# Optimization experiments

Hardware: AMD Instinct MI355X
Metric: run time of the kernel (lower is better)

## Reference

```python
import jax, jax.numpy as jnp
import numpy as np

KSIZE = 3
PAD = (KSIZE - 1) // 2
SIGMA = 0.15 * KSIZE + 0.35  # 0.8, used for BOTH spatial and range weights (as in source)


def gaussian_kernel(ksize, sigma):
    if sigma <= 0:
        sigma = 0.3 * ((ksize - 1) * 0.5 - 1) + 0.8
    xs = np.arange(ksize, dtype=np.float32) - ksize // 2
    k1 = np.exp(-xs ** 2 / (2.0 * sigma ** 2))
    k = k1[:, None] * k1[None, :]
    return jnp.asarray((k / k.sum()).astype(np.float32))


def setup_inputs() -> dict:
    key = jax.random.key(0)
    ks = jax.random.split(key, 5)
    B, C_in, H, W = 8, 256, 128, 128
    C2 = 128
    x1 = jax.random.normal(ks[0], (B, C_in, H, W), jnp.float32)
    x2 = jax.random.normal(ks[1], (B, C2, 2 * H, 2 * W), jnp.float32)
    # Conv2d(in_ch, 1, kernel_size=1): weight [out=1, in], bias [1]
    w1 = jax.random.normal(ks[2], (1, C_in), jnp.float32) / np.float32(np.sqrt(C_in))
    b1 = jnp.zeros((1,), jnp.float32)
    # ConvTranspose2d(1, 1, k=2, s=2): weight [2, 2], bias [1]
    wt = jax.random.normal(ks[3], (2, 2), jnp.float32) * 0.5
    bt = jnp.zeros((1,), jnp.float32)
    return {"x1": x1, "x2": x2, "w1": w1, "b1": b1, "wt": wt, "bt": bt}


def reference(x1, x2, w1, b1, wt, bt):
    # 1x1 conv: [B, C_in, H, W] -> [B, 1, H, W]
    y = jnp.einsum('bchw,oc->bohw', x1, w1) + b1[None, :, None, None]
    B, _, H, W = y.shape
    # ConvTranspose2d(1,1,k=2,s=2): out[2h+dh, 2w+dw] = y[h,w] * wt[dh,dw] + bt
    up = (y[:, :, :, None, :, None] * wt[None, None, None, :, None, :]).reshape(
        B, 1, 2 * H, 2 * W) + bt[None, :, None, None]
    Hu, Wu = 2 * H, 2 * W
    # reflect pad then extract ksize x ksize patches (unfold equivalent)
    xp = jnp.pad(up, ((0, 0), (0, 0), (PAD, PAD), (PAD, PAD)), mode='reflect')
    patches = jnp.stack(
        [xp[:, :, i:i + Hu, j:j + Wu] for i in range(KSIZE) for j in range(KSIZE)],
        axis=-1)  # [B, 1, Hu, Wu, K*K]
    w_space = gaussian_kernel(KSIZE, SIGMA).reshape(-1)  # [K*K]
    diff = patches - up[..., None]
    w_color = jnp.exp(-(diff ** 2) / (2.0 * SIGMA ** 2))
    weights = w_color * w_space  # joint bilateral weights
    filtered = (weights * patches).sum(-1) / weights.sum(-1)  # [B, 1, Hu, Wu]
    gate = jax.nn.sigmoid(filtered)
    return gate * x2 + x2
```

## Files before the change

kernel.cpp:

```cpp
#include <hip/hip_runtime.h>
#include <hip/hip_bf16.h>


#define B     8
#define CIN   256
#define H     128
#define W     128
#define C2    128
#define HU    256
#define WU    256

__global__ __launch_bounds__(256) void conv1x1_kernel(
    const float* __restrict__ x1, const float* __restrict__ w1,
    const float* __restrict__ b1, float* __restrict__ y)
{
    __shared__ float wsh[CIN];
    __shared__ float4 sred[256];
    int tid = threadIdx.x;
    wsh[tid] = w1[tid];
    __syncthreads();

    int b      = blockIdx.x >> 6;
    int hwbase = (blockIdx.x & 63) * 256;

    int q  = tid & 63;
    int cc = tid >> 6;

    const float4* p = (const float4*)(x1 + (size_t)b * CIN * H * W + hwbase) + q;
    const int cstride = H * W / 4;

    float4 acc = make_float4(0.f, 0.f, 0.f, 0.f);
    int c0 = cc * 64;
    #pragma unroll 8
    for (int k = 0; k < 64; ++k) {
        int c = c0 + k;
        float4 v = p[(size_t)c * cstride];
        float wv = wsh[c];
        acc.x += v.x * wv; acc.y += v.y * wv;
        acc.z += v.z * wv; acc.w += v.w * wv;
    }
    sred[tid] = acc;
    __syncthreads();

    if (cc == 0) {
        float4 a = sred[q], b2 = sred[q + 64], c2 = sred[q + 128], d2 = sred[q + 192];
        float bias = b1[0];
        float4 r;
        r.x = a.x + b2.x + c2.x + d2.x + bias;
        r.y = a.y + b2.y + c2.y + d2.y + bias;
        r.z = a.z + b2.z + c2.z + d2.z + bias;
        r.w = a.w + b2.w + c2.w + d2.w + bias;
        ((float4*)(y + (size_t)b * H * W + hwbase))[q] = r;
    }
}

__device__ __forceinline__ int refl(int i, int n) {
    return i < 0 ? -i : (i >= n ? 2 * n - 2 - i : i);
}

__global__ __launch_bounds__(256) void bilateral_gate_kernel(
    const float* __restrict__ y, const float* __restrict__ x2,
    const float* __restrict__ wt, const float* __restrict__ bt,
    float* __restrict__ out)
{
    __shared__ float scale_sh[WU];

    int hu = blockIdx.x & 255;
    int b  = blockIdx.x >> 8;
    int tid = threadIdx.x;

    {
        int wu = tid;
        const float* yb = y + (size_t)b * (H * W);
        float w00 = wt[0], w01 = wt[1], w10 = wt[2], w11 = wt[3];
        float btv = bt[0];

        float u[3][3];
        #pragma unroll
        for (int r = 0; r < 3; ++r) {
            int i  = refl(hu - 1 + r, HU);
            int iy = (i >> 1) * W;
            float wr0 = (i & 1) ? w10 : w00;
            float wr1 = (i & 1) ? w11 : w01;
            #pragma unroll
            for (int c = 0; c < 3; ++c) {
                int j = refl(wu - 1 + c, WU);
                u[r][c] = yb[iy + (j >> 1)] * ((j & 1) ? wr1 : wr0) + btv;
            }
        }

        const float inv2s2 = 0.78125f;
        const float e1 = expf(-inv2s2);
        float k1v[3] = { e1, 1.f, e1 };

        float ctr = u[1][1];
        float num = 0.f, den = 0.f;
        #pragma unroll
        for (int r = 0; r < 3; ++r) {
            #pragma unroll
            for (int c = 0; c < 3; ++c) {
                float pv = u[r][c];
                float d  = pv - ctr;
                float w  = expf(-(d * d) * inv2s2) * (k1v[r] * k1v[c]);
                num += w * pv;
                den += w;
            }
        }
        float f = num / den;
        float g = 1.f / (1.f + expf(-f));
        scale_sh[wu] = 1.f + g;
    }
    __syncthreads();

    int g  = tid & 63;
    int cc = tid >> 6;
    float4 sc = ((const float4*)scale_sh)[g];

    size_t base = (size_t)b * C2 * HU * WU + (size_t)hu * WU + (size_t)g * 4;
    const int cstride = HU * WU / 4;
    const float4* xp = (const float4*)(x2 + base) + (size_t)(cc * 32) * cstride;
    float4*       op = (float4*)(out + base)     + (size_t)(cc * 32) * cstride;

    #pragma unroll 8
    for (int k = 0; k < 32; ++k) {
        float4 v = xp[(size_t)k * cstride];
        v.x *= sc.x; v.y *= sc.y; v.z *= sc.z; v.w *= sc.w;
        op[(size_t)k * cstride] = v;
    }
}

extern "C" void kernel_launch(void* const* d_in, const int* in_sizes, int n_in,
                              void* d_out, int out_size, void* d_ws, size_t ws_size,
                              hipStream_t stream) {
    const float* x1 = (const float*)d_in[0];
    const float* x2 = (const float*)d_in[1];
    const float* w1 = (const float*)d_in[2];
    const float* b1 = (const float*)d_in[3];
    const float* wt = (const float*)d_in[4];
    const float* bt = (const float*)d_in[5];
    float* out = (float*)d_out;
    float* y   = (float*)d_ws;

    conv1x1_kernel<<<512, 256, 0, stream>>>(x1, w1, b1, y);
    bilateral_gate_kernel<<<B * HU, 256, 0, stream>>>(y, x2, wt, bt, out);
}
```

Before: 517.1 us.

## Split bilateral gate into gate-map kernel and flat grid-stride scaling stream

Moves the bilateral filter and sigmoid into a separate kernel that writes a per-pixel scale map to workspace. The multiply by x2 becomes a flat grid-stride float4 stream that reads x2 contiguously and fetches the matching scale entry, instead of each block walking 128 channel planes at a large stride. The aim is more sequential, bandwidth-friendly access on the dominant x2 read and write. In exchange it adds a kernel launch, a gate-map write and re-reads of the small map, which should mostly hit cache.

```diff
diff --git a/kernel.cpp b/kernel.cpp
--- a/kernel.cpp
+++ b/kernel.cpp
@@ -1,5 +1,4 @@
 #include <hip/hip_runtime.h>
-#include <hip/hip_bf16.h>
 
 
 #define B     8
@@ -58,74 +57,71 @@
     return i < 0 ? -i : (i >= n ? 2 * n - 2 - i : i);
 }
 
-__global__ __launch_bounds__(256) void bilateral_gate_kernel(
-    const float* __restrict__ y, const float* __restrict__ x2,
-    const float* __restrict__ wt, const float* __restrict__ bt,
+__global__ __launch_bounds__(256) void gate_map_kernel(
+    const float* __restrict__ y, const float* __restrict__ wt,
+    const float* __restrict__ bt, float* __restrict__ gmap)
+{
+    int hu = blockIdx.x & 255;
+    int b  = blockIdx.x >> 8;
+    int wu = threadIdx.x;
+
+    const float* yb = y + (size_t)b * (H * W);
+    float w00 = wt[0], w01 = wt[1], w10 = wt[2], w11 = wt[3];
+    float btv = bt[0];
+
+    float u[3][3];
+    #pragma unroll
+    for (int r = 0; r < 3; ++r) {
+        int i  = refl(hu - 1 + r, HU);
+        int iy = (i >> 1) * W;
+        float wr0 = (i & 1) ? w10 : w00;
+        float wr1 = (i & 1) ? w11 : w01;
+        #pragma unroll
+        for (int c = 0; c < 3; ++c) {
+            int j = refl(wu - 1 + c, WU);
+            u[r][c] = yb[iy + (j >> 1)] * ((j & 1) ? wr1 : wr0) + btv;
+        }
+    }
+
+    const float inv2s2 = 0.78125f;
+    const float e1 = expf(-inv2s2);
+    float k1v[3] = { e1, 1.f, e1 };
+
+    float ctr = u[1][1];
+    float num = 0.f, den = 0.f;
+    #pragma unroll
+    for (int r = 0; r < 3; ++r) {
+        #pragma unroll
+        for (int c = 0; c < 3; ++c) {
+            float pv = u[r][c];
+            float d  = pv - ctr;
+            float w  = expf(-(d * d) * inv2s2) * (k1v[r] * k1v[c]);
+            num += w * pv;
+            den += w;
+        }
+    }
+    float f = num / den;
+    float g = 1.f / (1.f + expf(-f));
+    gmap[(size_t)blockIdx.x * WU + wu] = 1.f + g;
+}
+
+__global__ __launch_bounds__(256) void scale_stream_kernel(
+    const float* __restrict__ x2, const float* __restrict__ gmap,
     float* __restrict__ out)
 {
-    __shared__ float scale_sh[WU];
+    const size_t total  = (size_t)B * C2 * HU * WU / 4;
+    const size_t stride = (size_t)gridDim.x * blockDim.x;
+    const float4* xp = (const float4*)x2;
+    const float4* gp = (const float4*)gmap;
+    float4*       op = (float4*)out;
 
-    int hu = blockIdx.x & 255;
-    int b  = blockIdx.x >> 8;
-    int tid = threadIdx.x;
-
-    {
-        int wu = tid;
-        const float* yb = y + (size_t)b * (H * W);
-        float w00 = wt[0], w01 = wt[1], w10 = wt[2], w11 = wt[3];
-        float btv = bt[0];
-
-        float u[3][3];
-        #pragma unroll
-        for (int r = 0; r < 3; ++r) {
-            int i  = refl(hu - 1 + r, HU);
-            int iy = (i >> 1) * W;
-            float wr0 = (i & 1) ? w10 : w00;
-            float wr1 = (i & 1) ? w11 : w01;
-            #pragma unroll
-            for (int c = 0; c < 3; ++c) {
-                int j = refl(wu - 1 + c, WU);
-                u[r][c] = yb[iy + (j >> 1)] * ((j & 1) ? wr1 : wr0) + btv;
-            }
-        }
-
-        const float inv2s2 = 0.78125f;
-        const float e1 = expf(-inv2s2);
-        float k1v[3] = { e1, 1.f, e1 };
-
-        float ctr = u[1][1];
-        float num = 0.f, den = 0.f;
-        #pragma unroll
-        for (int r = 0; r < 3; ++r) {
-            #pragma unroll
-            for (int c = 0; c < 3; ++c) {
-                float pv = u[r][c];
-                float d  = pv - ctr;
-                float w  = expf(-(d * d) * inv2s2) * (k1v[r] * k1v[c]);
-                num += w * pv;
-                den += w;
-            }
-        }
-        float f = num / den;
-        float g = 1.f / (1.f + expf(-f));
-        scale_sh[wu] = 1.f + g;
-    }
-    __syncthreads();
-
-    int g  = tid & 63;
-    int cc = tid >> 6;
-    float4 sc = ((const float4*)scale_sh)[g];
-
-    size_t base = (size_t)b * C2 * HU * WU + (size_t)hu * WU + (size_t)g * 4;
-    const int cstride = HU * WU / 4;
-    const float4* xp = (const float4*)(x2 + base) + (size_t)(cc * 32) * cstride;
-    float4*       op = (float4*)(out + base)     + (size_t)(cc * 32) * cstride;
-
-    #pragma unroll 8
-    for (int k = 0; k < 32; ++k) {
-        float4 v = xp[(size_t)k * cstride];
+    for (size_t idx = (size_t)blockIdx.x * blockDim.x + threadIdx.x;
+         idx < total; idx += stride) {
+        size_t gidx = ((idx >> 21) << 14) | (idx & 16383);
+        float4 sc = gp[gidx];
+        float4 v  = xp[idx];
         v.x *= sc.x; v.y *= sc.y; v.z *= sc.z; v.w *= sc.w;
-        op[(size_t)k * cstride] = v;
+        op[idx] = v;
     }
 }
 
@@ -136,11 +132,13 @@
     const float* x2 = (const float*)d_in[1];
     const float* w1 = (const float*)d_in[2];
     const float* b1 = (const float*)d_in[3];
+    const float* bt = (const float*)d_in[5];
     const float* wt = (const float*)d_in[4];
-    const float* bt = (const float*)d_in[5];
-    float* out = (float*)d_out;
-    float* y   = (float*)d_ws;
+    float* out  = (float*)d_out;
+    float* y    = (float*)d_ws;
+    float* gmap = (float*)d_ws + (size_t)H * W * B;
 
     conv1x1_kernel<<<512, 256, 0, stream>>>(x1, w1, b1, y);
-    bilateral_gate_kernel<<<B * HU, 256, 0, stream>>>(y, x2, wt, bt, out);
+    gate_map_kernel<<<B * HU, 256, 0, stream>>>(y, wt, bt, gmap);
+    scale_stream_kernel<<<2048, 256, 0, stream>>>(x2, gmap, out);
 }
```

After: 519.9 us. About the same (+0.5%).
